# Kernel optimization log

Hardware: AMD Instinct MI355X
Metric: run time of the kernel (lower is better)

The kernel has to match this reference:

```python
import jax, jax.numpy as jnp
import numpy as np

GRID = 2
SPAN = 2.0
EMBED = 64
HIDDEN = 128
PRED_LEN = 12
N = 1024
T = 8
SCENE_SIZE = 64


def _social_pool(ht, pos, scene, active):
    """ht: [N,H], pos: [N,2], scene: [N] int, active: [N] bool -> [N, GRID*GRID, H].
    Vectorized equivalent of the per-scene scatter_add pooling: pairwise mask over
    same-scene, active, within-area, non-self pairs; bin neighbor hidden states."""
    n = ht.shape[0]
    half = SPAN / 2.0
    eps = 0.01
    rel = pos[None, :, :] - pos[:, None, :]  # rel[i,j] = pos_j - pos_i
    within = ((rel[..., 0] < half - eps) & (rel[..., 0] > -half + eps)
              & (rel[..., 1] < half - eps) & (rel[..., 1] > -half + eps))
    pair = (within & (~jnp.eye(n, dtype=bool))
            & (scene[:, None] == scene[None, :])
            & active[:, None] & active[None, :])
    cell = SPAN / GRID
    gidx = jnp.floor((rel + half) / cell).astype(jnp.int32)
    gid = jnp.clip(gidx[..., 0] * GRID + gidx[..., 1], 0, GRID * GRID - 1)
    onehot = jax.nn.one_hot(gid, GRID * GRID, dtype=ht.dtype) * pair[..., None].astype(ht.dtype)
    # pooled[i,g,h] = sum_j onehot[i,j,g] * ht[j,h]
    return jnp.einsum('ijg,jh->igh', onehot, ht)


def _lstm_step(x, h, c, Wih, Whh, bih, bhh):
    z = x @ Wih.T + bih + h @ Whh.T + bhh
    i, f, g, o = jnp.split(z, 4, axis=-1)
    c_new = jax.nn.sigmoid(f) * c + jax.nn.sigmoid(i) * jnp.tanh(g)
    h_new = jax.nn.sigmoid(o) * jnp.tanh(c_new)
    return h_new, c_new


def setup_inputs() -> dict:
    key = jax.random.key(0)
    ks = jax.random.split(key, 16)
    past_traj = jax.random.uniform(ks[0], (N, T, 2), dtype=jnp.float32) * 8.0
    past_traj_rel = jax.random.normal(ks[1], (N, T, 2), dtype=jnp.float32)
    past_traj_timestamp_mask = jnp.ones((N, T), dtype=jnp.int32)
    is_predictable = jnp.ones((N, 1), dtype=jnp.int32)
    same_scene_mask = (jnp.arange(N, dtype=jnp.int32) // SCENE_SIZE).reshape(N, 1)

    def lin(k, fan_out, fan_in):
        b = 1.0 / np.sqrt(fan_in)
        return jax.random.uniform(k, (fan_out, fan_in), jnp.float32, -b, b)

    pos_W = lin(ks[2], EMBED, 2)
    pos_b = jnp.zeros((EMBED,), jnp.float32)
    soc_W = lin(ks[3], EMBED, GRID * GRID * HIDDEN)
    soc_b = jnp.zeros((EMBED,), jnp.float32)
    Wih = lin(ks[4], 4 * HIDDEN, 2 * EMBED)
    Whh = lin(ks[5], 4 * HIDDEN, HIDDEN)
    bih = jnp.zeros((4 * HIDDEN,), jnp.float32)
    bhh = jnp.zeros((4 * HIDDEN,), jnp.float32)
    h0 = jax.random.normal(ks[6], (HIDDEN,), jnp.float32) * 0.1
    c0 = jax.random.normal(ks[7], (HIDDEN,), jnp.float32) * 0.1
    pred_W = lin(ks[8], 5, HIDDEN)
    pred_b = jnp.zeros((5,), jnp.float32)
    return {
        'past_traj': past_traj, 'past_traj_rel': past_traj_rel,
        'past_traj_timestamp_mask': past_traj_timestamp_mask,
        'is_predictable': is_predictable, 'same_scene_mask': same_scene_mask,
        'pos_W': pos_W, 'pos_b': pos_b, 'soc_W': soc_W, 'soc_b': soc_b,
        'Wih': Wih, 'Whh': Whh, 'bih': bih, 'bhh': bhh,
        'h0': h0, 'c0': c0, 'pred_W': pred_W, 'pred_b': pred_b,
    }


def reference(past_traj, past_traj_rel, past_traj_timestamp_mask, is_predictable,
              same_scene_mask, pos_W, pos_b, soc_W, soc_b, Wih, Whh, bih, bhh,
              h0, c0, pred_W, pred_b):
    n = past_traj.shape[0]
    scene = same_scene_mask[:, 0]
    ht = jnp.broadcast_to(h0[None, :], (n, HIDDEN))
    ct = jnp.broadcast_to(c0[None, :], (n, HIDDEN))

    def obs_step(carry, inp):
        ht, ct = carry
        point, rel, m = inp  # [N,2], [N,2], [N]
        active = m == 1
        pooled = _social_pool(ht, point, scene, active)  # [N,G^2,H]
        et = jax.nn.relu(rel @ pos_W.T + pos_b)
        at = jax.nn.relu(pooled.reshape(n, -1) @ soc_W.T + soc_b)
        x = jnp.concatenate([et, at], axis=-1)
        h_new, c_new = _lstm_step(x, ht, ct, Wih, Whh, bih, bhh)
        ht = jnp.where(active[:, None], h_new, ht)
        ct = jnp.where(active[:, None], c_new, ct)
        return (ht, ct), None

    obs_inp = (jnp.moveaxis(past_traj, 1, 0), jnp.moveaxis(past_traj_rel, 1, 0),
               jnp.moveaxis(past_traj_timestamp_mask, 1, 0))
    (ht, ct), _ = jax.lax.scan(obs_step, (ht, ct), obs_inp)

    pred_active = past_traj_timestamp_mask[:, -1] == 1
    pos0 = past_traj[:, -1, :]

    def pred_step(carry, _):
        ht, ct, pos = carry
        out = ht @ pred_W.T + pred_b  # [N,5]
        rel = out[:, :2]
        pos = pos + rel
        pooled = _social_pool(ht, pos, scene, pred_active)
        et = jax.nn.relu(rel @ pos_W.T + pos_b)
        at = jax.nn.relu(pooled.reshape(n, -1) @ soc_W.T + soc_b)
        x = jnp.concatenate([et, at], axis=-1)
        h_new, c_new = _lstm_step(x, ht, ct, Wih, Whh, bih, bhh)
        ht = jnp.where(pred_active[:, None], h_new, ht)
        ct = jnp.where(pred_active[:, None], c_new, ct)
        return (ht, ct, pos), (out, pos)

    (_, _, _), (outs, trajs) = jax.lax.scan(pred_step, (ht, ct, pos0), None, length=PRED_LEN)
    pred_out_all = jnp.where(pred_active[:, None, None], jnp.moveaxis(outs, 0, 1), 0.0)
    pred_traj_all = jnp.where(pred_active[:, None, None], jnp.moveaxis(trajs, 0, 1), 0.0)
    # is_predictable is all-ones in this setup, so the final boolean filter is identity
    return pred_out_all, pred_traj_all
```

## Files before the change

kernel.cpp:

```cpp
#include <hip/hip_runtime.h>

#define NAGENT 64
#define HID    128
#define TOBS   8
#define PREDL  12
#define NTHR   512
#define XP     264
#define PP     264
#define S2P    264

typedef __attribute__((ext_vector_type(8))) short bf16x8;
typedef __attribute__((ext_vector_type(4))) float f32x4;
typedef __attribute__((ext_vector_type(4))) int   i32x4;
typedef __attribute__((ext_vector_type(2))) unsigned int u32x2;

__device__ __forceinline__ unsigned short f2bf(float f) {
    unsigned int x = __float_as_uint(f);
    unsigned int r = (x + 0x7fffu + ((x >> 16) & 1u)) >> 16;
    return (unsigned short)r;
}
__device__ __forceinline__ float bf2f(unsigned short u) {
    return __uint_as_float(((unsigned int)u) << 16);
}
__device__ __forceinline__ float sigmf(float x) {
    return __builtin_amdgcn_rcpf(1.0f + __expf(-x));
}
__device__ __forceinline__ float tanhf_fast(float x) {
    x = fminf(fmaxf(x, -15.0f), 15.0f);
    float e = __expf(2.0f * x);
    return (e - 1.0f) * __builtin_amdgcn_rcpf(e + 1.0f);
}

__global__ void prep_weights(const float* __restrict__ Wih, const float* __restrict__ Whh,
                             const float* __restrict__ socW, const float* __restrict__ predW,
                             unsigned short* __restrict__ wd, unsigned short* __restrict__ wb,
                             unsigned short* __restrict__ wp) {
    int idx = blockIdx.x * 256 + threadIdx.x;
    if (idx < 131072) {
        int e = idx & 7, l = (idx >> 3) & 63, t = idx >> 9;
        int kt = t & 7, nt = t >> 3;
        int k = kt * 32 + ((l >> 4) << 3) + e;
        int n = nt * 16 + (l & 15);
        float v = (k < 128) ? Wih[n * 128 + k] : Whh[n * 128 + (k - 128)];
        wd[idx] = f2bf(v);
    } else if (idx < 163840) {
        int i2 = idx - 131072;
        int e = i2 & 7, l = (i2 >> 3) & 63, t = i2 >> 9;
        int kt = t & 3, nt = t >> 2;
        int k = kt * 32 + ((l >> 4) << 3) + e;
        int r = nt * 16 + (l & 15);
        wb[i2] = f2bf(socW[(r >> 2) * 512 + (r & 3) * 128 + k]);
    } else if (idx < 167936) {
        int i3 = idx - 163840;
        int e = i3 & 7, l = (i3 >> 3) & 63, f = i3 >> 9;
        int kt = f & 3, half = f >> 2;
        int k = kt * 32 + ((l >> 4) << 3) + e;
        int n = l & 15;
        float v = (n < 5) ? predW[n * 128 + k] : 0.0f;
        unsigned short hi = f2bf(v);
        wp[i3] = half ? f2bf(v - bf2f(hi)) : hi;
    }
}

__global__ __launch_bounds__(NTHR, 2) void social_lstm_mfma(
    const float* __restrict__ past_traj, const float* __restrict__ past_traj_rel,
    const int* __restrict__ ts_mask, const int* __restrict__ scene_in,
    const float* __restrict__ pos_W, const float* __restrict__ pos_b,
    const float* __restrict__ soc_b,
    const float* __restrict__ bih, const float* __restrict__ bhh,
    const float* __restrict__ h0, const float* __restrict__ c0,
    const float* __restrict__ pred_b,
    const unsigned short* __restrict__ wd, const unsigned short* __restrict__ wb,
    const unsigned short* __restrict__ wp,
    float* __restrict__ out)
{
    __shared__ __align__(16) unsigned short sh_X[NAGENT][XP];
    __shared__ __align__(16) unsigned short sh_P[NAGENT][PP];
    __shared__ __align__(16) unsigned short sh_S2[NAGENT][S2P];
    __shared__ float sh_px[NAGENT], sh_py[NAGENT], sh_rx[NAGENT], sh_ry[NAGENT];
    __shared__ float sh_o[5][NAGENT];
    __shared__ __align__(16) int sh_act[NAGENT];
    __shared__ int sh_scene[NAGENT];

    const int tid  = threadIdx.x;
    const int lane = tid & 63;
    const int wv   = __builtin_amdgcn_readfirstlane(tid >> 6);
    const int gbase = blockIdx.x * NAGENT;
    const int c16 = lane & 15;
    const int q4  = lane >> 4;
    const int dim = wv * 16 + c16;

    bf16x8 wdf[4][8];
    {
        const bf16x8* wdv = (const bf16x8*)wd;
        #pragma unroll
        for (int g = 0; g < 4; ++g)
            #pragma unroll
            for (int kt = 0; kt < 8; ++kt)
                wdf[g][kt] = wdv[(((g * 8 + wv) * 8) + kt) * 64 + lane];
    }
    const float bs0 = bih[0 * 128 + dim] + bhh[0 * 128 + dim];
    const float bs1 = bih[1 * 128 + dim] + bhh[1 * 128 + dim];
    const float bs2 = bih[2 * 128 + dim] + bhh[2 * 128 + dim];
    const float bs3 = bih[3 * 128 + dim] + bhh[3 * 128 + dim];
    float c_reg[16];
    {
        const float cz = c0[dim];
        #pragma unroll
        for (int u = 0; u < 16; ++u) c_reg[u] = cz;
    }
    for (int p = tid; p < NAGENT * HID; p += NTHR) {
        int a = p >> 7, d = p & 127;
        sh_X[a][128 + d] = f2bf(h0[d]);
    }
    if (tid < NAGENT) {
        sh_scene[tid] = scene_in[gbase + tid];
        const int ig = gbase + tid;
        sh_px[tid] = past_traj[(ig * TOBS + 0) * 2 + 0];
        sh_py[tid] = past_traj[(ig * TOBS + 0) * 2 + 1];
        sh_rx[tid] = past_traj_rel[(ig * TOBS + 0) * 2 + 0];
        sh_ry[tid] = past_traj_rel[(ig * TOBS + 0) * 2 + 1];
        sh_act[tid] = (ts_mask[ig * TOBS + 0] == 1) ? 1 : 0;
    }
    __syncthreads();

    for (int step = 0; step < TOBS + PREDL; ++step) {
        if (step >= TOBS) {
            if (wv < 4) {
                const bf16x8* wpv = (const bf16x8*)wp;
                f32x4 pa = (f32x4){0.f, 0.f, 0.f, 0.f};
                #pragma unroll
                for (int kt = 0; kt < 4; ++kt) {
                    const bf16x8 a = *(const bf16x8*)&sh_X[wv * 16 + c16][128 + kt * 32 + q4 * 8];
                    pa = __builtin_amdgcn_mfma_f32_16x16x32_bf16(a, wpv[kt * 64 + lane], pa, 0, 0, 0);
                    pa = __builtin_amdgcn_mfma_f32_16x16x32_bf16(a, wpv[(4 + kt) * 64 + lane], pa, 0, 0, 0);
                }
                if (c16 < 5) {
                    const float pb = pred_b[c16];
                    #pragma unroll
                    for (int rr = 0; rr < 4; ++rr)
                        sh_o[c16][wv * 16 + q4 * 4 + rr] = pa[rr] + pb;
                }
            }
            __syncthreads();
            if (tid < NAGENT) {
                const int i = tid;
                const float rx = sh_o[0][i], ry = sh_o[1][i];
                const float px = sh_px[i] + rx, py = sh_py[i] + ry;
                sh_px[i] = px; sh_py[i] = py;
                sh_rx[i] = rx; sh_ry[i] = ry;
                const float m = sh_act[i] ? 1.0f : 0.0f;
                const int p = step - TOBS;
                const int ig = gbase + i;
                float* po = out + (ig * PREDL + p) * 5;
                #pragma unroll
                for (int q = 0; q < 5; ++q) po[q] = m * sh_o[q][i];
                float* pt = out + 61440 + (ig * PREDL + p) * 2;
                pt[0] = m * px; pt[1] = m * py;
            }
            __syncthreads();
        }

        #pragma unroll
        for (int it = 0; it < 8; ++it) {
            const int p = it * NTHR + tid;
            const int i = p >> 6, j = p & 63;
            const float dx = sh_px[j] - sh_px[i];
            const float dy = sh_py[j] - sh_py[i];
            const bool within = (dx < 0.99f) & (dx > -0.99f) & (dy < 0.99f) & (dy > -0.99f);
            const bool pair = within && (i != j) && (sh_scene[i] == sh_scene[j])
                              && sh_act[i] && sh_act[j];
            const int gid = ((dx >= 0.f) ? 2 : 0) + ((dy >= 0.f) ? 1 : 0);
            unsigned int w0 = 0, w1 = 0;
            if (pair) {
                if (gid == 0) w0 = 0x3f80u;
                else if (gid == 1) w0 = 0x3f800000u;
                else if (gid == 2) w1 = 0x3f80u;
                else w1 = 0x3f800000u;
            }
            u32x2 w; w[0] = w0; w[1] = w1;
            *(u32x2*)&sh_P[i][j * 4] = w;
        }
        {
            const float rx = sh_rx[lane], ry = sh_ry[lane];
            bf16x8 ev;
            #pragma unroll
            for (int u = 0; u < 8; ++u) {
                const int e = wv * 8 + u;
                ev[u] = (short)f2bf(fmaxf(pos_b[e] + rx * pos_W[2 * e] + ry * pos_W[2 * e + 1], 0.f));
            }
            *(bf16x8*)&sh_X[lane][wv * 8] = ev;
        }
        {
            const bf16x8* wbv = (const bf16x8*)wb;
            bf16x8 wbf[2][4];
            #pragma unroll
            for (int s = 0; s < 2; ++s)
                #pragma unroll
                for (int kt = 0; kt < 4; ++kt)
                    wbf[s][kt] = wbv[((2 * wv + s) * 4 + kt) * 64 + lane];
            #pragma unroll
            for (int mj = 0; mj < 4; ++mj) {
                bf16x8 a[4];
                #pragma unroll
                for (int kt = 0; kt < 4; ++kt)
                    a[kt] = *(const bf16x8*)&sh_X[mj * 16 + c16][128 + kt * 32 + q4 * 8];
                f32x4 ac[2];
                ac[0] = (f32x4){0.f, 0.f, 0.f, 0.f};
                ac[1] = (f32x4){0.f, 0.f, 0.f, 0.f};
                #pragma unroll
                for (int kt = 0; kt < 4; ++kt) {
                    ac[0] = __builtin_amdgcn_mfma_f32_16x16x32_bf16(a[kt], wbf[0][kt], ac[0], 0, 0, 0);
                    ac[1] = __builtin_amdgcn_mfma_f32_16x16x32_bf16(a[kt], wbf[1][kt], ac[1], 0, 0, 0);
                }
                #pragma unroll
                for (int s = 0; s < 2; ++s) {
                    const int r = (2 * wv + s) * 16 + c16;
                    const int e = r >> 2, g = r & 3;
                    #pragma unroll
                    for (int rr = 0; rr < 4; ++rr)
                        sh_S2[e][(mj * 16 + q4 * 4 + rr) * 4 + g] = f2bf(ac[s][rr]);
                }
            }
        }
        __syncthreads();

        {
            const int mt = wv & 3, np = wv >> 2;
            f32x4 ac[2];
            ac[0] = (f32x4){0.f, 0.f, 0.f, 0.f};
            ac[1] = (f32x4){0.f, 0.f, 0.f, 0.f};
            #pragma unroll
            for (int kt = 0; kt < 8; ++kt) {
                const bf16x8 a = *(const bf16x8*)&sh_P[mt * 16 + c16][kt * 32 + q4 * 8];
                ac[0] = __builtin_amdgcn_mfma_f32_16x16x32_bf16(
                    a, *(const bf16x8*)&sh_S2[(2 * np) * 16 + c16][kt * 32 + q4 * 8], ac[0], 0, 0, 0);
                ac[1] = __builtin_amdgcn_mfma_f32_16x16x32_bf16(
                    a, *(const bf16x8*)&sh_S2[(2 * np + 1) * 16 + c16][kt * 32 + q4 * 8], ac[1], 0, 0, 0);
            }
            #pragma unroll
            for (int s = 0; s < 2; ++s) {
                const int e = (2 * np + s) * 16 + c16;
                const float sb = soc_b[e];
                #pragma unroll
                for (int rr = 0; rr < 4; ++rr)
                    sh_X[mt * 16 + q4 * 4 + rr][64 + e] = f2bf(fmaxf(ac[s][rr] + sb, 0.f));
            }
        }
        __syncthreads();

        float hn_st[16];
        unsigned int hm = 0;
        #pragma unroll
        for (int mj = 0; mj < 4; ++mj) {
            bf16x8 a[8];
            #pragma unroll
            for (int kt = 0; kt < 8; ++kt)
                a[kt] = *(const bf16x8*)&sh_X[mj * 16 + c16][kt * 32 + q4 * 8];
            f32x4 acc[4];
            #pragma unroll
            for (int g = 0; g < 4; ++g) acc[g] = (f32x4){0.f, 0.f, 0.f, 0.f};
            #pragma unroll
            for (int kt = 0; kt < 8; ++kt)
                #pragma unroll
                for (int g = 0; g < 4; ++g)
                    acc[g] = __builtin_amdgcn_mfma_f32_16x16x32_bf16(a[kt], wdf[g][kt], acc[g], 0, 0, 0);
            const i32x4 a4 = *(const i32x4*)&sh_act[mj * 16 + q4 * 4];
            #pragma unroll
            for (int rr = 0; rr < 4; ++rr) {
                const float zi = acc[0][rr] + bs0;
                const float zf = acc[1][rr] + bs1;
                const float zg = acc[2][rr] + bs2;
                const float zo = acc[3][rr] + bs3;
                const float cold = c_reg[mj * 4 + rr];
                const float cn = sigmf(zf) * cold + sigmf(zi) * tanhf_fast(zg);
                const float hn = sigmf(zo) * tanhf_fast(cn);
                const bool act = a4[rr] != 0;
                c_reg[mj * 4 + rr] = act ? cn : cold;
                hn_st[mj * 4 + rr] = hn;
                hm |= (act ? 1u : 0u) << (mj * 4 + rr);
            }
        }
        __syncthreads();

        #pragma unroll
        for (int u = 0; u < 16; ++u) {
            if (hm & (1u << u)) {
                const int mj = u >> 2, rr = u & 3;
                sh_X[mj * 16 + q4 * 4 + rr][128 + dim] = f2bf(hn_st[u]);
            }
        }
        if (step + 1 < TOBS && tid < NAGENT) {
            const int ig = gbase + tid;
            sh_px[tid] = past_traj[(ig * TOBS + step + 1) * 2 + 0];
            sh_py[tid] = past_traj[(ig * TOBS + step + 1) * 2 + 1];
            sh_rx[tid] = past_traj_rel[(ig * TOBS + step + 1) * 2 + 0];
            sh_ry[tid] = past_traj_rel[(ig * TOBS + step + 1) * 2 + 1];
            sh_act[tid] = (ts_mask[ig * TOBS + step + 1] == 1) ? 1 : 0;
        }
        __syncthreads();
    }
}

extern "C" void kernel_launch(void* const* d_in, const int* in_sizes, int n_in,
                              void* d_out, int out_size, void* d_ws, size_t ws_size,
                              hipStream_t stream) {
    (void)in_sizes; (void)n_in; (void)out_size; (void)ws_size;
    unsigned short* wd = (unsigned short*)d_ws;
    unsigned short* wb = wd + 131072;
    unsigned short* wp = wb + 32768;
    prep_weights<<<656, 256, 0, stream>>>(
        (const float*)d_in[9], (const float*)d_in[10],
        (const float*)d_in[7], (const float*)d_in[15], wd, wb, wp);
    social_lstm_mfma<<<16, NTHR, 0, stream>>>(
        (const float*)d_in[0],
        (const float*)d_in[1],
        (const int*)  d_in[2],
        (const int*)  d_in[4],
        (const float*)d_in[5],
        (const float*)d_in[6],
        (const float*)d_in[8],
        (const float*)d_in[11],
        (const float*)d_in[12],
        (const float*)d_in[13],
        (const float*)d_in[14],
        (const float*)d_in[16],
        wd, wb, wp,
        (float*)d_out);
}
```

Before: 358.6 us.

## Double block to 1024 threads and split agent tiles across wave groups

Raises the block size from 512 to 1024 threads and splits the agent rows between two groups of 8 waves, so each wave handles half the M-tiles in the social, pooling and LSTM gate GEMMs. The LSTM weight fragments are no longer kept in registers for the whole kernel; they are reloaded from global memory (L2) on every step, while the social-weight fragments are hoisted out of the step loop. The pooling mask layout and the S2 layout change to a grid-major ordering and use packed stores. The aim is more parallelism per serial timestep; the cost is repeated weight traffic and a launch bound that allows only one block resident per CU.

```diff
diff --git a/kernel.cpp b/kernel.cpp
--- a/kernel.cpp
+++ b/kernel.cpp
@@ -4,15 +4,15 @@
 #define HID    128
 #define TOBS   8
 #define PREDL  12
-#define NTHR   512
+#define NTHR   1024
 #define XP     264
 #define PP     264
 #define S2P    264
 
 typedef __attribute__((ext_vector_type(8))) short bf16x8;
+typedef __attribute__((ext_vector_type(4))) short bf16x4;
 typedef __attribute__((ext_vector_type(4))) float f32x4;
 typedef __attribute__((ext_vector_type(4))) int   i32x4;
-typedef __attribute__((ext_vector_type(2))) unsigned int u32x2;
 
 __device__ __forceinline__ unsigned short f2bf(float f) {
     unsigned int x = __float_as_uint(f);
@@ -62,7 +62,7 @@
     }
 }
 
-__global__ __launch_bounds__(NTHR, 2) void social_lstm_mfma(
+__global__ __launch_bounds__(NTHR) void social_lstm_mfma(
     const float* __restrict__ past_traj, const float* __restrict__ past_traj_rel,
     const int* __restrict__ ts_mask, const int* __restrict__ scene_in,
     const float* __restrict__ pos_W, const float* __restrict__ pos_b,
@@ -88,26 +88,29 @@
     const int gbase = blockIdx.x * NAGENT;
     const int c16 = lane & 15;
     const int q4  = lane >> 4;
-    const int dim = wv * 16 + c16;
-
-    bf16x8 wdf[4][8];
+
+    const int sub8 = wv & 7;
+    const int mjg  = wv >> 3;
+    const int dim  = sub8 * 16 + c16;
+
+    bf16x8 wbf[2][4];
     {
-        const bf16x8* wdv = (const bf16x8*)wd;
+        const bf16x8* wbv = (const bf16x8*)wb;
         #pragma unroll
-        for (int g = 0; g < 4; ++g)
-            #pragma unroll
-            for (int kt = 0; kt < 8; ++kt)
-                wdf[g][kt] = wdv[(((g * 8 + wv) * 8) + kt) * 64 + lane];
+        for (int s = 0; s < 2; ++s)
+            #pragma unroll
+            for (int kt = 0; kt < 4; ++kt)
+                wbf[s][kt] = wbv[((2 * sub8 + s) * 4 + kt) * 64 + lane];
     }
     const float bs0 = bih[0 * 128 + dim] + bhh[0 * 128 + dim];
     const float bs1 = bih[1 * 128 + dim] + bhh[1 * 128 + dim];
     const float bs2 = bih[2 * 128 + dim] + bhh[2 * 128 + dim];
     const float bs3 = bih[3 * 128 + dim] + bhh[3 * 128 + dim];
-    float c_reg[16];
+    float c_reg[8];
     {
         const float cz = c0[dim];
         #pragma unroll
-        for (int u = 0; u < 16; ++u) c_reg[u] = cz;
+        for (int u = 0; u < 8; ++u) c_reg[u] = cz;
     }
     for (int p = tid; p < NAGENT * HID; p += NTHR) {
         int a = p >> 7, d = p & 127;
@@ -162,7 +165,7 @@
         }
 
         #pragma unroll
-        for (int it = 0; it < 8; ++it) {
+        for (int it = 0; it < 4; ++it) {
             const int p = it * NTHR + tid;
             const int i = p >> 6, j = p & 63;
             const float dx = sh_px[j] - sh_px[i];
@@ -171,17 +174,12 @@
             const bool pair = within && (i != j) && (sh_scene[i] == sh_scene[j])
                               && sh_act[i] && sh_act[j];
             const int gid = ((dx >= 0.f) ? 2 : 0) + ((dy >= 0.f) ? 1 : 0);
-            unsigned int w0 = 0, w1 = 0;
-            if (pair) {
-                if (gid == 0) w0 = 0x3f80u;
-                else if (gid == 1) w0 = 0x3f800000u;
-                else if (gid == 2) w1 = 0x3f80u;
-                else w1 = 0x3f800000u;
-            }
-            u32x2 w; w[0] = w0; w[1] = w1;
-            *(u32x2*)&sh_P[i][j * 4] = w;
-        }
-        {
+            #pragma unroll
+            for (int g = 0; g < 4; ++g)
+                sh_P[i][g * 64 + j] = (pair && gid == g) ? (unsigned short)0x3f80
+                                                         : (unsigned short)0;
+        }
+        if (wv < 8) {
             const float rx = sh_rx[lane], ry = sh_ry[lane];
             bf16x8 ev;
             #pragma unroll
@@ -192,102 +190,96 @@
             *(bf16x8*)&sh_X[lane][wv * 8] = ev;
         }
         {
-            const bf16x8* wbv = (const bf16x8*)wb;
-            bf16x8 wbf[2][4];
-            #pragma unroll
-            for (int s = 0; s < 2; ++s)
-                #pragma unroll
-                for (int kt = 0; kt < 4; ++kt)
-                    wbf[s][kt] = wbv[((2 * wv + s) * 4 + kt) * 64 + lane];
-            #pragma unroll
-            for (int mj = 0; mj < 4; ++mj) {
-                bf16x8 a[4];
-                #pragma unroll
-                for (int kt = 0; kt < 4; ++kt)
-                    a[kt] = *(const bf16x8*)&sh_X[mj * 16 + c16][128 + kt * 32 + q4 * 8];
-                f32x4 ac[2];
-                ac[0] = (f32x4){0.f, 0.f, 0.f, 0.f};
-                ac[1] = (f32x4){0.f, 0.f, 0.f, 0.f};
-                #pragma unroll
-                for (int kt = 0; kt < 4; ++kt) {
-                    ac[0] = __builtin_amdgcn_mfma_f32_16x16x32_bf16(a[kt], wbf[0][kt], ac[0], 0, 0, 0);
-                    ac[1] = __builtin_amdgcn_mfma_f32_16x16x32_bf16(a[kt], wbf[1][kt], ac[1], 0, 0, 0);
-                }
+            f32x4 bac[2][2];
+            #pragma unroll
+            for (int a = 0; a < 2; ++a) { bac[a][0] = (f32x4){0,0,0,0}; bac[a][1] = (f32x4){0,0,0,0}; }
+            #pragma unroll
+            for (int kt = 0; kt < 4; ++kt) {
+                const bf16x8 a0 = *(const bf16x8*)&sh_X[(2 * mjg + 0) * 16 + c16][128 + kt * 32 + q4 * 8];
+                const bf16x8 a1 = *(const bf16x8*)&sh_X[(2 * mjg + 1) * 16 + c16][128 + kt * 32 + q4 * 8];
                 #pragma unroll
                 for (int s = 0; s < 2; ++s) {
-                    const int r = (2 * wv + s) * 16 + c16;
+                    bac[0][s] = __builtin_amdgcn_mfma_f32_16x16x32_bf16(a0, wbf[s][kt], bac[0][s], 0, 0, 0);
+                    bac[1][s] = __builtin_amdgcn_mfma_f32_16x16x32_bf16(a1, wbf[s][kt], bac[1][s], 0, 0, 0);
+                }
+            }
+            #pragma unroll
+            for (int mjl = 0; mjl < 2; ++mjl)
+                #pragma unroll
+                for (int s = 0; s < 2; ++s) {
+                    const int r = (2 * sub8 + s) * 16 + c16;
                     const int e = r >> 2, g = r & 3;
+                    bf16x4 pk;
                     #pragma unroll
-                    for (int rr = 0; rr < 4; ++rr)
-                        sh_S2[e][(mj * 16 + q4 * 4 + rr) * 4 + g] = f2bf(ac[s][rr]);
-                }
-            }
+                    for (int i = 0; i < 4; ++i) pk[i] = (short)f2bf(bac[mjl][s][i]);
+                    *(bf16x4*)&sh_S2[e][g * 64 + (2 * mjg + mjl) * 16 + q4 * 4] = pk;
+                }
         }
         __syncthreads();
 
         {
-            const int mt = wv & 3, np = wv >> 2;
-            f32x4 ac[2];
-            ac[0] = (f32x4){0.f, 0.f, 0.f, 0.f};
-            ac[1] = (f32x4){0.f, 0.f, 0.f, 0.f};
+            const int mt = wv & 3, nt = wv >> 2;
+            f32x4 cac = (f32x4){0.f, 0.f, 0.f, 0.f};
             #pragma unroll
             for (int kt = 0; kt < 8; ++kt) {
                 const bf16x8 a = *(const bf16x8*)&sh_P[mt * 16 + c16][kt * 32 + q4 * 8];
-                ac[0] = __builtin_amdgcn_mfma_f32_16x16x32_bf16(
-                    a, *(const bf16x8*)&sh_S2[(2 * np) * 16 + c16][kt * 32 + q4 * 8], ac[0], 0, 0, 0);
-                ac[1] = __builtin_amdgcn_mfma_f32_16x16x32_bf16(
-                    a, *(const bf16x8*)&sh_S2[(2 * np + 1) * 16 + c16][kt * 32 + q4 * 8], ac[1], 0, 0, 0);
-            }
-            #pragma unroll
-            for (int s = 0; s < 2; ++s) {
-                const int e = (2 * np + s) * 16 + c16;
-                const float sb = soc_b[e];
-                #pragma unroll
-                for (int rr = 0; rr < 4; ++rr)
-                    sh_X[mt * 16 + q4 * 4 + rr][64 + e] = f2bf(fmaxf(ac[s][rr] + sb, 0.f));
-            }
+                const bf16x8 b = *(const bf16x8*)&sh_S2[nt * 16 + c16][kt * 32 + q4 * 8];
+                cac = __builtin_amdgcn_mfma_f32_16x16x32_bf16(a, b, cac, 0, 0, 0);
+            }
+            const int e = nt * 16 + c16;
+            const float sb = soc_b[e];
+            #pragma unroll
+            for (int rr = 0; rr < 4; ++rr)
+                sh_X[mt * 16 + q4 * 4 + rr][64 + e] = f2bf(fmaxf(cac[rr] + sb, 0.f));
         }
         __syncthreads();
 
-        float hn_st[16];
+        float hn_st[8];
         unsigned int hm = 0;
+        {
+            const bf16x8* wdv = (const bf16x8*)wd;
+            f32x4 acc[2][4];
+            #pragma unroll
+            for (int a = 0; a < 2; ++a)
+                #pragma unroll
+                for (int g = 0; g < 4; ++g) acc[a][g] = (f32x4){0.f, 0.f, 0.f, 0.f};
+            #pragma unroll 2
+            for (int kt = 0; kt < 8; ++kt) {
+                const bf16x8 a0 = *(const bf16x8*)&sh_X[(2 * mjg + 0) * 16 + c16][kt * 32 + q4 * 8];
+                const bf16x8 a1 = *(const bf16x8*)&sh_X[(2 * mjg + 1) * 16 + c16][kt * 32 + q4 * 8];
+                #pragma unroll
+                for (int g = 0; g < 4; ++g) {
+                    const bf16x8 b = wdv[((g * 8 + sub8) * 8 + kt) * 64 + lane];
+                    acc[0][g] = __builtin_amdgcn_mfma_f32_16x16x32_bf16(a0, b, acc[0][g], 0, 0, 0);
+                    acc[1][g] = __builtin_amdgcn_mfma_f32_16x16x32_bf16(a1, b, acc[1][g], 0, 0, 0);
+                }
+            }
+            #pragma unroll
+            for (int mjl = 0; mjl < 2; ++mjl) {
+                const i32x4 a4 = *(const i32x4*)&sh_act[(2 * mjg + mjl) * 16 + q4 * 4];
+                #pragma unroll
+                for (int rr = 0; rr < 4; ++rr) {
+                    const float zi = acc[mjl][0][rr] + bs0;
+                    const float zf = acc[mjl][1][rr] + bs1;
+                    const float zg = acc[mjl][2][rr] + bs2;
+                    const float zo = acc[mjl][3][rr] + bs3;
+                    const float cold = c_reg[mjl * 4 + rr];
+                    const float cn = sigmf(zf) * cold + sigmf(zi) * tanhf_fast(zg);
+                    const float hn = sigmf(zo) * tanhf_fast(cn);
+                    const bool act = a4[rr] != 0;
+                    c_reg[mjl * 4 + rr] = act ? cn : cold;
+                    hn_st[mjl * 4 + rr] = hn;
+                    hm |= (act ? 1u : 0u) << (mjl * 4 + rr);
+                }
+            }
+        }
+        __syncthreads();
+
         #pragma unroll
-        for (int mj = 0; mj < 4; ++mj) {
-            bf16x8 a[8];
-            #pragma unroll
-            for (int kt = 0; kt < 8; ++kt)
-                a[kt] = *(const bf16x8*)&sh_X[mj * 16 + c16][kt * 32 + q4 * 8];
-            f32x4 acc[4];
-            #pragma unroll
-            for (int g = 0; g < 4; ++g) acc[g] = (f32x4){0.f, 0.f, 0.f, 0.f};
-            #pragma unroll
-            for (int kt = 0; kt < 8; ++kt)
-                #pragma unroll
-                for (int g = 0; g < 4; ++g)
-                    acc[g] = __builtin_amdgcn_mfma_f32_16x16x32_bf16(a[kt], wdf[g][kt], acc[g], 0, 0, 0);
-            const i32x4 a4 = *(const i32x4*)&sh_act[mj * 16 + q4 * 4];
-            #pragma unroll
-            for (int rr = 0; rr < 4; ++rr) {
-                const float zi = acc[0][rr] + bs0;
-                const float zf = acc[1][rr] + bs1;
-                const float zg = acc[2][rr] + bs2;
-                const float zo = acc[3][rr] + bs3;
-                const float cold = c_reg[mj * 4 + rr];
-                const float cn = sigmf(zf) * cold + sigmf(zi) * tanhf_fast(zg);
-                const float hn = sigmf(zo) * tanhf_fast(cn);
-                const bool act = a4[rr] != 0;
-                c_reg[mj * 4 + rr] = act ? cn : cold;
-                hn_st[mj * 4 + rr] = hn;
-                hm |= (act ? 1u : 0u) << (mj * 4 + rr);
-            }
-        }
-        __syncthreads();
-
-        #pragma unroll
-        for (int u = 0; u < 16; ++u) {
+        for (int u = 0; u < 8; ++u) {
             if (hm & (1u << u)) {
-                const int mj = u >> 2, rr = u & 3;
-                sh_X[mj * 16 + q4 * 4 + rr][128 + dim] = f2bf(hn_st[u]);
+                const int mjl = u >> 2, rr = u & 3;
+                sh_X[(2 * mjg + mjl) * 16 + q4 * 4 + rr][128 + dim] = f2bf(hn_st[u]);
             }
         }
         if (step + 1 < TOBS && tid < NAGENT) {
```

After: 323.1 us. 9.9% less time.
